# Performance work log

Hardware: AMD Instinct MI355X
Metric: run time of the kernel (lower is better)

Reference implementation:

```python
import jax, jax.numpy as jnp
import numpy as np

B, S, D, H = 2, 2048, 1024, 16
HD = D // H  # 64
LN_EPS = 1e-5


def setup_inputs() -> dict:
    key = jax.random.key(0)
    ks = jax.random.split(key, 5)
    hidden_states = jax.random.normal(ks[0], (B, S, D), dtype=jnp.float32)
    attention_mask = jnp.zeros((B, 1, 1, S), dtype=jnp.float32)  # additive mask
    # LayerNorm params
    ln_gamma = jnp.ones((D,), dtype=jnp.float32)
    ln_beta = jnp.zeros((D,), dtype=jnp.float32)
    # Q/K/V projections, no bias; stored as [in, out]
    sc = 1.0 / np.sqrt(D)
    Wq = jax.random.normal(ks[1], (D, D), dtype=jnp.float32) * sc
    Wk = jax.random.normal(ks[2], (D, D), dtype=jnp.float32) * sc
    Wv = jax.random.normal(ks[3], (D, D), dtype=jnp.float32) * sc
    return {"hidden_states": hidden_states, "attention_mask": attention_mask,
            "ln_gamma": ln_gamma, "ln_beta": ln_beta, "Wq": Wq, "Wk": Wk, "Wv": Wv}


def _layernorm(x, g, b):
    mu = jnp.mean(x, axis=-1, keepdims=True)
    var = jnp.mean(jnp.square(x - mu), axis=-1, keepdims=True)
    return (x - mu) * jax.lax.rsqrt(var + LN_EPS) * g + b


def reference(hidden_states, attention_mask, ln_gamma, ln_beta, Wq, Wk, Wv):
    h = _layernorm(hidden_states, ln_gamma, ln_beta)          # [B,S,D]
    # project and split heads: [B,S,D] -> [B,H,S,HD]
    def split_heads(x):
        return x.reshape(B, S, H, HD).transpose(0, 2, 1, 3)
    q = split_heads(h @ Wq)
    k = split_heads(h @ Wk)
    v = split_heads(h @ Wv)
    scores = jnp.einsum('bhqd,bhkd->bhqk', q, k) / jnp.sqrt(jnp.float32(HD))
    scores = scores + attention_mask                           # additive mask broadcast
    probs = jax.nn.softmax(scores, axis=-1)                    # dropout p=0 -> identity
    ctx = jnp.einsum('bhqk,bhkd->bhqd', probs, v)              # [B,H,S,HD]
    ctx = ctx.transpose(0, 2, 1, 3).reshape(B, S, H * HD)      # [B,S,D]
    return ctx
```

## Files before the change

kernel.cpp:

```cpp
#include <hip/hip_runtime.h>
#include <hip/hip_bf16.h>
#include <cstdint>

#define B_ 2
#define S_ 2048
#define D_ 1024
#define H_ 16
#define HD_ 64
#define M_ (B_*S_)

#define LOG2E 1.4426950408889634f
#define C1_ (0.125f * LOG2E)

typedef unsigned short u16;
typedef __bf16 bf16x8 __attribute__((ext_vector_type(8)));
typedef u16 u16x8 __attribute__((ext_vector_type(8)));
typedef float f32x4 __attribute__((ext_vector_type(4)));
typedef float f32x16 __attribute__((ext_vector_type(16)));
typedef int i32x4 __attribute__((ext_vector_type(4)));

static __device__ __forceinline__ u16 f2bu(float f) {
  __bf16 b = (__bf16)f;
  return __builtin_bit_cast(unsigned short, b);
}

static __device__ __forceinline__ int cvtpk(float a, float b) {
  int r;
  asm("v_cvt_pk_bf16_f32 %0, %1, %2" : "=v"(r) : "v"(a), "v"(b));
  return r;
}
static __device__ __forceinline__ void plswap(int &x, int &y) {
  asm("v_permlane32_swap_b32 %0, %1" : "+v"(x), "+v"(y));
}

#define GLOAD16(g, l) __builtin_amdgcn_global_load_lds( \
    (__attribute__((address_space(1))) void*)(g), \
    (__attribute__((address_space(3))) void*)(l), 16, 0, 0)

__global__ __launch_bounds__(256) void ln_kernel(const float* __restrict__ x,
    const float* __restrict__ g, const float* __restrict__ be, u16* __restrict__ h) {
  const int row = blockIdx.x;
  const int t = threadIdx.x;
  float4 v = reinterpret_cast<const float4*>(x + (size_t)row * D_)[t];
  float s = v.x + v.y + v.z + v.w;
  float sq = v.x*v.x + v.y*v.y + v.z*v.z + v.w*v.w;
  #pragma unroll
  for (int off = 32; off >= 1; off >>= 1) {
    s  += __shfl_down(s, off);
    sq += __shfl_down(sq, off);
  }
  __shared__ float red[8];
  const int wave = t >> 6, lane = t & 63;
  if (lane == 0) { red[wave] = s; red[4 + wave] = sq; }
  __syncthreads();
  if (t == 0) {
    float ts = red[0]+red[1]+red[2]+red[3];
    float tq = red[4]+red[5]+red[6]+red[7];
    float mu = ts * (1.0f / D_);
    red[0] = mu;
    red[1] = rsqrtf(tq * (1.0f / D_) - mu*mu + 1e-5f);
  }
  __syncthreads();
  const float mu = red[0], rs = red[1];
  float4 gg = reinterpret_cast<const float4*>(g)[t];
  float4 bb = reinterpret_cast<const float4*>(be)[t];
  ushort4 o;
  o.x = f2bu((v.x - mu) * rs * gg.x + bb.x);
  o.y = f2bu((v.y - mu) * rs * gg.y + bb.y);
  o.z = f2bu((v.z - mu) * rs * gg.z + bb.z);
  o.w = f2bu((v.w - mu) * rs * gg.w + bb.w);
  reinterpret_cast<ushort4*>(h + (size_t)row * D_)[t] = o;
}

__global__ __launch_bounds__(256) void wt_kernel(const float* __restrict__ W0,
    const float* __restrict__ W1, const float* __restrict__ W2, u16* __restrict__ wt) {
  const int z = blockIdx.z;
  const float* W = (z == 0) ? W0 : ((z == 1) ? W1 : W2);
  u16* out = wt + (size_t)z * D_ * D_;
  __shared__ float tile[32][33];
  const int n0 = blockIdx.x * 32, k0 = blockIdx.y * 32;
  const int tx = threadIdx.x, ty = threadIdx.y;
  #pragma unroll
  for (int j = 0; j < 4; ++j)
    tile[ty + 8*j][tx] = W[(size_t)(k0 + ty + 8*j) * D_ + n0 + tx];
  __syncthreads();
  #pragma unroll
  for (int j = 0; j < 4; ++j)
    out[(size_t)(n0 + ty + 8*j) * D_ + k0 + tx] = f2bu(tile[tx][ty + 8*j]);
}

__global__ __launch_bounds__(256) void qkv_gemm(const u16* __restrict__ hbuf,
    const u16* __restrict__ wt, u16* __restrict__ qkv) {
  const int z = blockIdx.z;
  const u16* Bt = wt + (size_t)z * D_ * D_;
  u16* outp = qkv + (size_t)z * (B_*H_*S_*HD_);
  __shared__ __align__(16) u16 As[128 * 32];
  __shared__ __align__(16) u16 Bs[128 * 32];
  const int t = threadIdx.x, lane = t & 63, wave = t >> 6;
  const int row0 = blockIdx.y * 128, col0 = blockIdx.x * 128;
  const int wm = wave >> 1, wn = wave & 1;
  f32x4 acc[4][4] = {};
  const int schunk = (t & 3) ^ ((t >> 3) & 3);
  const u16* ag = hbuf + (size_t)(row0 + (t >> 2)) * D_ + schunk * 8;
  const u16* bg = Bt   + (size_t)(col0 + (t >> 2)) * D_ + schunk * 8;
  u16* lA = &As[wave * 512];
  u16* lB = &Bs[wave * 512];
  const char* Ac = (const char*)As;
  const char* Bc = (const char*)Bs;
  const int cbase = (((lane >> 4) ^ ((lane >> 1) & 3)) << 4);

  for (int k0 = 0; k0 < D_; k0 += 32) {
    GLOAD16(ag + k0,           lA);
    GLOAD16(ag + k0 + 64 * D_, lA + 2048);
    GLOAD16(bg + k0,           lB);
    GLOAD16(bg + k0 + 64 * D_, lB + 2048);
    __syncthreads();
    bf16x8 af[4], bfr[4];
    #pragma unroll
    for (int m = 0; m < 4; ++m)
      af[m] = *reinterpret_cast<const bf16x8*>(Ac + (wm*64 + m*16 + (lane & 15)) * 64 + cbase);
    #pragma unroll
    for (int n = 0; n < 4; ++n)
      bfr[n] = *reinterpret_cast<const bf16x8*>(Bc + (wn*64 + n*16 + (lane & 15)) * 64 + cbase);
    #pragma unroll
    for (int m = 0; m < 4; ++m) {
      #pragma unroll
      for (int n = 0; n < 4; ++n)
        acc[m][n] = __builtin_amdgcn_mfma_f32_16x16x32_bf16(af[m], bfr[n], acc[m][n], 0, 0, 0);
    }
    __syncthreads();
  }
  #pragma unroll
  for (int m = 0; m < 4; ++m) {
    #pragma unroll
    for (int n = 0; n < 4; ++n) {
      const int gcol = col0 + wn*64 + n*16 + (lane & 15);
      const int hI = gcol >> 6, dI = gcol & 63;
      #pragma unroll
      for (int r = 0; r < 4; ++r) {
        const int grow = row0 + wm*64 + m*16 + (lane >> 4) * 4 + r;
        const int bI = grow >> 11, sI = grow & (S_ - 1);
        size_t idx;
        if (z == 2) idx = ((size_t)(bI * H_ + hI) * HD_ + dI) * S_ + sI;
        else        idx = ((size_t)(bI * H_ + hI) * S_ + sI) * HD_ + dI;
        outp[idx] = f2bu(acc[m][n][r]);
      }
    }
  }
}

static __device__ __forceinline__ void sm_pack(
    const f32x16& s, const float* __restrict__ mrow, int hf,
    float& dm, float& lsum, f32x16& o0, f32x16& o1,
    bf16x8& pfA, bf16x8& pfB) {
  float4 m0 = *reinterpret_cast<const float4*>(mrow + 4*hf);
  float4 m1 = *reinterpret_cast<const float4*>(mrow + 8 + 4*hf);
  float4 m2 = *reinterpret_cast<const float4*>(mrow + 16 + 4*hf);
  float4 m3 = *reinterpret_cast<const float4*>(mrow + 24 + 4*hf);
  float zb[16];
  #pragma unroll
  for (int r = 0; r < 4; ++r) {
    zb[r]      = s[r]      * C1_ + ((const float*)&m0)[r];
    zb[r + 4]  = s[r + 4]  * C1_ + ((const float*)&m1)[r];
    zb[r + 8]  = s[r + 8]  * C1_ + ((const float*)&m2)[r];
    zb[r + 12] = s[r + 12] * C1_ + ((const float*)&m3)[r];
  }
  float a0 = fmaxf(fmaxf(zb[0], zb[1]), zb[2]);
  float a1 = fmaxf(fmaxf(zb[3], zb[4]), zb[5]);
  float a2 = fmaxf(fmaxf(zb[6], zb[7]), zb[8]);
  float a3 = fmaxf(fmaxf(zb[9], zb[10]), zb[11]);
  float a4 = fmaxf(fmaxf(zb[12], zb[13]), zb[14]);
  float tm = fmaxf(fmaxf(fmaxf(a0, a1), fmaxf(a2, a3)), fmaxf(a4, zb[15]));
  tm = fmaxf(tm, __shfl_xor(tm, 32));
  if (__builtin_expect(__any(tm > dm + 8.0f), 0)) {
    float dnew = fmaxf(dm, tm - 8.0f);
    float sf = __builtin_amdgcn_exp2f(dm - dnew);
    lsum *= sf; o0 = o0 * sf; o1 = o1 * sf; dm = dnew;
  }
  float p[16];
  #pragma unroll
  for (int r = 0; r < 16; ++r) p[r] = __builtin_amdgcn_exp2f(zb[r] - dm);
  float s01 = (p[0] + p[1]) + (p[2] + p[3]);
  float s23 = (p[4] + p[5]) + (p[6] + p[7]);
  float s45 = (p[8] + p[9]) + (p[10] + p[11]);
  float s67 = (p[12] + p[13]) + (p[14] + p[15]);
  float rs = (s01 + s23) + (s45 + s67);
  rs += __shfl_xor(rs, 32);
  lsum += rs;
  int pk01 = cvtpk(p[0], p[1]),   pk23 = cvtpk(p[2], p[3]);
  int pk45 = cvtpk(p[4], p[5]),   pk67 = cvtpk(p[6], p[7]);
  int pk89 = cvtpk(p[8], p[9]),   pkAB = cvtpk(p[10], p[11]);
  int pkCD = cvtpk(p[12], p[13]), pkEF = cvtpk(p[14], p[15]);
  plswap(pk01, pk45); plswap(pk23, pk67);
  plswap(pk89, pkCD); plswap(pkAB, pkEF);
  i32x4 c0 = {pk01, pk23, pk45, pk67};
  i32x4 c1 = {pk89, pkAB, pkCD, pkEF};
  pfA = __builtin_bit_cast(bf16x8, c0);
  pfB = __builtin_bit_cast(bf16x8, c1);
}

__global__ __launch_bounds__(256, 2) void attn_kernel(const u16* __restrict__ qkv,
    const float* __restrict__ mask, float* __restrict__ out) {
  const int bid = blockIdx.x;
  const int x = bid & 7, rr = bid >> 3;
  const int j = rr & 15;
  const int pidx = x + ((rr >> 4) << 3);
  const int hI = pidx & 15, bI = pidx >> 4;
  const size_t plane = (size_t)pidx * (S_ * HD_);
  const u16* Qp  = qkv + plane;
  const u16* Kp  = qkv + (size_t)(B_*H_*S_*HD_) + plane;
  const u16* Vtp = qkv + 2*(size_t)(B_*H_*S_*HD_) + plane;

  const int t = threadIdx.x, lane = t & 63, wave = t >> 6;
  const int cl = lane & 31, hf = lane >> 5;
  const int swz = (cl & 7) << 4;

  __shared__ __align__(16) u16 KsBuf[2][64 * 64];
  __shared__ __align__(16) u16 VsBuf[2][64 * 64];
  __shared__ float maskLds[S_];

  #pragma unroll
  for (int i = 0; i < 2; ++i) {
    float4 mv = reinterpret_cast<const float4*>(mask + (size_t)bI * S_)[t + i*256];
    float4 sm = {mv.x * LOG2E - 8.0f, mv.y * LOG2E - 8.0f,
                 mv.z * LOG2E - 8.0f, mv.w * LOG2E - 8.0f};
    reinterpret_cast<float4*>(maskLds)[t + i*256] = sm;
  }

  const int q0 = j * 128 + wave * 32;
  bf16x8 qf[4];
  #pragma unroll
  for (int d = 0; d < 4; ++d)
    qf[d] = *reinterpret_cast<const bf16x8*>(
        Qp + (size_t)(q0 + cl) * HD_ + d * 16 + hf * 8);

  const int sr = t >> 3;
  const int scol = (((t & 7) * 16) ^ ((sr & 7) << 4)) >> 1;
  const u16* kSrc = Kp  + (size_t)sr * HD_ + scol;
  const u16* vSrc = Vtp + (size_t)sr * S_  + scol;
  const int L0 = wave * 512, L1 = 2048 + wave * 512;

  f32x16 oacc0 = {}, oacc1 = {};
  float dm = 0.f, lsum = 0.f;

  GLOAD16(kSrc,                  &KsBuf[0][L0]);
  GLOAD16(kSrc + 32 * HD_,       &KsBuf[0][L1]);
  GLOAD16(vSrc,                  &VsBuf[0][L0]);
  GLOAD16(vSrc + 32 * (size_t)S_, &VsBuf[0][L1]);
  int cur = 0;

  for (int kv0 = 0; kv0 < S_; kv0 += 64) {
    __syncthreads();
    if (kv0 + 64 < S_) {
      const u16* kn = kSrc + (size_t)(kv0 + 64) * HD_;
      const u16* vn = vSrc + (kv0 + 64);
      GLOAD16(kn,                   &KsBuf[cur ^ 1][L0]);
      GLOAD16(kn + 32 * HD_,        &KsBuf[cur ^ 1][L1]);
      GLOAD16(vn,                   &VsBuf[cur ^ 1][L0]);
      GLOAD16(vn + 32 * (size_t)S_, &VsBuf[cur ^ 1][L1]);
    }
    const char* Ks = (const char*)KsBuf[cur];
    const char* Vs = (const char*)VsBuf[cur];

    f32x16 s0 = {}, s1 = {};
    __builtin_amdgcn_s_setprio(1);
    #pragma unroll
    for (int d = 0; d < 4; ++d) {
      bf16x8 kf = *reinterpret_cast<const bf16x8*>(
          Ks + cl * 128 + ((d * 32 + hf * 16) ^ swz));
      s0 = __builtin_amdgcn_mfma_f32_32x32x16_bf16(kf, qf[d], s0, 0, 0, 0);
    }
    #pragma unroll
    for (int d = 0; d < 4; ++d) {
      bf16x8 kf = *reinterpret_cast<const bf16x8*>(
          Ks + (32 + cl) * 128 + ((d * 32 + hf * 16) ^ swz));
      s1 = __builtin_amdgcn_mfma_f32_32x32x16_bf16(kf, qf[d], s1, 0, 0, 0);
    }
    __builtin_amdgcn_s_setprio(0);

    bf16x8 pA, pB;
    sm_pack(s0, maskLds + kv0, hf, dm, lsum, oacc0, oacc1, pA, pB);
    __builtin_amdgcn_s_setprio(1);
    {
      bf16x8 vf;
      vf = *reinterpret_cast<const bf16x8*>(Vs + cl * 128 + ((hf * 16) ^ swz));
      oacc0 = __builtin_amdgcn_mfma_f32_32x32x16_bf16(vf, pA, oacc0, 0, 0, 0);
      vf = *reinterpret_cast<const bf16x8*>(Vs + (32 + cl) * 128 + ((hf * 16) ^ swz));
      oacc1 = __builtin_amdgcn_mfma_f32_32x32x16_bf16(vf, pA, oacc1, 0, 0, 0);
      vf = *reinterpret_cast<const bf16x8*>(Vs + cl * 128 + ((32 + hf * 16) ^ swz));
      oacc0 = __builtin_amdgcn_mfma_f32_32x32x16_bf16(vf, pB, oacc0, 0, 0, 0);
      vf = *reinterpret_cast<const bf16x8*>(Vs + (32 + cl) * 128 + ((32 + hf * 16) ^ swz));
      oacc1 = __builtin_amdgcn_mfma_f32_32x32x16_bf16(vf, pB, oacc1, 0, 0, 0);
    }
    __builtin_amdgcn_s_setprio(0);
    sm_pack(s1, maskLds + kv0 + 32, hf, dm, lsum, oacc0, oacc1, pA, pB);
    __builtin_amdgcn_s_setprio(1);
    {
      bf16x8 vf;
      vf = *reinterpret_cast<const bf16x8*>(Vs + cl * 128 + ((64 + hf * 16) ^ swz));
      oacc0 = __builtin_amdgcn_mfma_f32_32x32x16_bf16(vf, pA, oacc0, 0, 0, 0);
      vf = *reinterpret_cast<const bf16x8*>(Vs + (32 + cl) * 128 + ((64 + hf * 16) ^ swz));
      oacc1 = __builtin_amdgcn_mfma_f32_32x32x16_bf16(vf, pA, oacc1, 0, 0, 0);
      vf = *reinterpret_cast<const bf16x8*>(Vs + cl * 128 + ((96 + hf * 16) ^ swz));
      oacc0 = __builtin_amdgcn_mfma_f32_32x32x16_bf16(vf, pB, oacc0, 0, 0, 0);
      vf = *reinterpret_cast<const bf16x8*>(Vs + (32 + cl) * 128 + ((96 + hf * 16) ^ swz));
      oacc1 = __builtin_amdgcn_mfma_f32_32x32x16_bf16(vf, pB, oacc1, 0, 0, 0);
    }
    __builtin_amdgcn_s_setprio(0);
    cur ^= 1;
  }

  const float rinv = 1.0f / lsum;
  float* orow = out + ((size_t)bI * S_ + q0 + cl) * D_ + hI * HD_;
  #pragma unroll
  for (int jj = 0; jj < 4; ++jj) {
    float4 o0 = {oacc0[4*jj] * rinv, oacc0[4*jj+1] * rinv, oacc0[4*jj+2] * rinv, oacc0[4*jj+3] * rinv};
    float4 o1 = {oacc1[4*jj] * rinv, oacc1[4*jj+1] * rinv, oacc1[4*jj+2] * rinv, oacc1[4*jj+3] * rinv};
    *reinterpret_cast<float4*>(orow + 8*jj + 4*hf)      = o0;
    *reinterpret_cast<float4*>(orow + 32 + 8*jj + 4*hf) = o1;
  }
}

extern "C" void kernel_launch(void* const* d_in, const int* in_sizes, int n_in,
                              void* d_out, int out_size, void* d_ws, size_t ws_size,
                              hipStream_t stream) {
  const float* x     = (const float*)d_in[0];
  const float* mask  = (const float*)d_in[1];
  const float* gamma = (const float*)d_in[2];
  const float* beta  = (const float*)d_in[3];
  const float* Wq    = (const float*)d_in[4];
  const float* Wk    = (const float*)d_in[5];
  const float* Wv    = (const float*)d_in[6];
  float* out = (float*)d_out;

  char* ws = (char*)d_ws;
  u16* hbuf = (u16*)ws;
  u16* wt   = (u16*)(ws + (size_t)M_*D_*2);
  u16* qkv  = (u16*)(ws + (size_t)M_*D_*2 + 3ull*D_*D_*2);

  hipLaunchKernelGGL(ln_kernel, dim3(M_), dim3(256), 0, stream, x, gamma, beta, hbuf);
  hipLaunchKernelGGL(wt_kernel, dim3(32, 32, 3), dim3(32, 8), 0, stream, Wq, Wk, Wv, wt);
  hipLaunchKernelGGL(qkv_gemm, dim3(8, 32, 3), dim3(256), 0, stream, hbuf, wt, qkv);
  hipLaunchKernelGGL(attn_kernel, dim3(512), dim3(256), 0, stream, qkv, mask, out);
}
```

Measured before the change: 111.0 us.

## Load K/V fragments directly from global into registers, dropping LDS staging

The attention kernel no longer stages K and V tiles through double-buffered shared memory with per-iteration barriers. Each wave loads its own MFMA operand fragments straight from global memory, with K prefetched one tile ahead in registers. The softmax scale is folded into the Q projection epilogue, and the cross-half row-sum shuffle is deferred to the end, so it only runs when the rescale branch fires. This removes LDS traffic and barriers but raises register pressure and relies on cache hits for K/V reuse across the four waves.

```diff
diff --git a/kernel.cpp b/kernel.cpp
--- a/kernel.cpp
+++ b/kernel.cpp
@@ -130,6 +130,7 @@
     }
     __syncthreads();
   }
+  const float scl = (z == 0) ? C1_ : 1.0f;
   #pragma unroll
   for (int m = 0; m < 4; ++m) {
     #pragma unroll
@@ -143,27 +144,23 @@
         size_t idx;
         if (z == 2) idx = ((size_t)(bI * H_ + hI) * HD_ + dI) * S_ + sI;
         else        idx = ((size_t)(bI * H_ + hI) * S_ + sI) * HD_ + dI;
-        outp[idx] = f2bu(acc[m][n][r]);
+        outp[idx] = f2bu(acc[m][n][r] * scl);
       }
     }
   }
 }
 
 static __device__ __forceinline__ void sm_pack(
-    const f32x16& s, const float* __restrict__ mrow, int hf,
+    const f32x16& s, const float4* __restrict__ mk,
     float& dm, float& lsum, f32x16& o0, f32x16& o1,
     bf16x8& pfA, bf16x8& pfB) {
-  float4 m0 = *reinterpret_cast<const float4*>(mrow + 4*hf);
-  float4 m1 = *reinterpret_cast<const float4*>(mrow + 8 + 4*hf);
-  float4 m2 = *reinterpret_cast<const float4*>(mrow + 16 + 4*hf);
-  float4 m3 = *reinterpret_cast<const float4*>(mrow + 24 + 4*hf);
   float zb[16];
   #pragma unroll
   for (int r = 0; r < 4; ++r) {
-    zb[r]      = s[r]      * C1_ + ((const float*)&m0)[r];
-    zb[r + 4]  = s[r + 4]  * C1_ + ((const float*)&m1)[r];
-    zb[r + 8]  = s[r + 8]  * C1_ + ((const float*)&m2)[r];
-    zb[r + 12] = s[r + 12] * C1_ + ((const float*)&m3)[r];
+    zb[r]      = s[r]      + ((const float*)&mk[0])[r];
+    zb[r + 4]  = s[r + 4]  + ((const float*)&mk[1])[r];
+    zb[r + 8]  = s[r + 8]  + ((const float*)&mk[2])[r];
+    zb[r + 12] = s[r + 12] + ((const float*)&mk[3])[r];
   }
   float a0 = fmaxf(fmaxf(zb[0], zb[1]), zb[2]);
   float a1 = fmaxf(fmaxf(zb[3], zb[4]), zb[5]);
@@ -171,9 +168,9 @@
   float a3 = fmaxf(fmaxf(zb[9], zb[10]), zb[11]);
   float a4 = fmaxf(fmaxf(zb[12], zb[13]), zb[14]);
   float tm = fmaxf(fmaxf(fmaxf(a0, a1), fmaxf(a2, a3)), fmaxf(a4, zb[15]));
-  tm = fmaxf(tm, __shfl_xor(tm, 32));
   if (__builtin_expect(__any(tm > dm + 8.0f), 0)) {
-    float dnew = fmaxf(dm, tm - 8.0f);
+    float tp = fmaxf(tm, __shfl_xor(tm, 32));
+    float dnew = fmaxf(dm, tp - 8.0f);
     float sf = __builtin_amdgcn_exp2f(dm - dnew);
     lsum *= sf; o0 = o0 * sf; o1 = o1 * sf; dm = dnew;
   }
@@ -184,9 +181,7 @@
   float s23 = (p[4] + p[5]) + (p[6] + p[7]);
   float s45 = (p[8] + p[9]) + (p[10] + p[11]);
   float s67 = (p[12] + p[13]) + (p[14] + p[15]);
-  float rs = (s01 + s23) + (s45 + s67);
-  rs += __shfl_xor(rs, 32);
-  lsum += rs;
+  lsum += (s01 + s23) + (s45 + s67);
   int pk01 = cvtpk(p[0], p[1]),   pk23 = cvtpk(p[2], p[3]);
   int pk45 = cvtpk(p[4], p[5]),   pk67 = cvtpk(p[6], p[7]);
   int pk89 = cvtpk(p[8], p[9]),   pkAB = cvtpk(p[10], p[11]);
@@ -213,12 +208,8 @@
 
   const int t = threadIdx.x, lane = t & 63, wave = t >> 6;
   const int cl = lane & 31, hf = lane >> 5;
-  const int swz = (cl & 7) << 4;
-
-  __shared__ __align__(16) u16 KsBuf[2][64 * 64];
-  __shared__ __align__(16) u16 VsBuf[2][64 * 64];
+
   __shared__ float maskLds[S_];
-
   #pragma unroll
   for (int i = 0; i < 2; ++i) {
     float4 mv = reinterpret_cast<const float4*>(mask + (size_t)bI * S_)[t + i*256];
@@ -233,83 +224,77 @@
   for (int d = 0; d < 4; ++d)
     qf[d] = *reinterpret_cast<const bf16x8*>(
         Qp + (size_t)(q0 + cl) * HD_ + d * 16 + hf * 8);
-
-  const int sr = t >> 3;
-  const int scol = (((t & 7) * 16) ^ ((sr & 7) << 4)) >> 1;
-  const u16* kSrc = Kp  + (size_t)sr * HD_ + scol;
-  const u16* vSrc = Vtp + (size_t)sr * S_  + scol;
-  const int L0 = wave * 512, L1 = 2048 + wave * 512;
+  __syncthreads();
+
+  const u16* kbase = Kp  + (size_t)cl * HD_ + hf * 8;
+  const u16* vbase = Vtp + (size_t)cl * S_  + hf * 8;
 
   f32x16 oacc0 = {}, oacc1 = {};
   float dm = 0.f, lsum = 0.f;
 
-  GLOAD16(kSrc,                  &KsBuf[0][L0]);
-  GLOAD16(kSrc + 32 * HD_,       &KsBuf[0][L1]);
-  GLOAD16(vSrc,                  &VsBuf[0][L0]);
-  GLOAD16(vSrc + 32 * (size_t)S_, &VsBuf[0][L1]);
-  int cur = 0;
-
-  for (int kv0 = 0; kv0 < S_; kv0 += 64) {
-    __syncthreads();
-    if (kv0 + 64 < S_) {
-      const u16* kn = kSrc + (size_t)(kv0 + 64) * HD_;
-      const u16* vn = vSrc + (kv0 + 64);
-      GLOAD16(kn,                   &KsBuf[cur ^ 1][L0]);
-      GLOAD16(kn + 32 * HD_,        &KsBuf[cur ^ 1][L1]);
-      GLOAD16(vn,                   &VsBuf[cur ^ 1][L0]);
-      GLOAD16(vn + 32 * (size_t)S_, &VsBuf[cur ^ 1][L1]);
+  bf16x8 kf[2][8];
+  #pragma unroll
+  for (int s = 0; s < 2; ++s)
+    #pragma unroll
+    for (int d = 0; d < 4; ++d)
+      kf[0][s*4+d] = *reinterpret_cast<const bf16x8*>(kbase + (size_t)(s*32) * HD_ + d*16);
+
+  for (int it = 0; it < 16; ++it) {
+    #pragma unroll
+    for (int h = 0; h < 2; ++h) {
+      const int tt = 2*it + h;
+      const int kv0 = tt * 64;
+      float4 mk0[4], mk1[4];
+      #pragma unroll
+      for (int i = 0; i < 4; ++i) {
+        mk0[i] = *reinterpret_cast<const float4*>(&maskLds[kv0 + 8*i + 4*hf]);
+        mk1[i] = *reinterpret_cast<const float4*>(&maskLds[kv0 + 32 + 8*i + 4*hf]);
+      }
+      bf16x8 vf[8];
+      #pragma unroll
+      for (int s = 0; s < 2; ++s) {
+        vf[s*4+0] = *reinterpret_cast<const bf16x8*>(vbase + kv0 + s*32);
+        vf[s*4+1] = *reinterpret_cast<const bf16x8*>(vbase + 32*(size_t)S_ + kv0 + s*32);
+        vf[s*4+2] = *reinterpret_cast<const bf16x8*>(vbase + kv0 + s*32 + 16);
+        vf[s*4+3] = *reinterpret_cast<const bf16x8*>(vbase + 32*(size_t)S_ + kv0 + s*32 + 16);
+      }
+      f32x16 s0 = {}, s1 = {};
+      __builtin_amdgcn_s_setprio(1);
+      #pragma unroll
+      for (int d = 0; d < 4; ++d)
+        s0 = __builtin_amdgcn_mfma_f32_32x32x16_bf16(kf[h][d], qf[d], s0, 0, 0, 0);
+      #pragma unroll
+      for (int d = 0; d < 4; ++d)
+        s1 = __builtin_amdgcn_mfma_f32_32x32x16_bf16(kf[h][4+d], qf[d], s1, 0, 0, 0);
+      __builtin_amdgcn_s_setprio(0);
+      {
+        const int tn = (tt < 31) ? tt + 1 : 31;
+        const u16* kn = kbase + (size_t)(tn * 64) * HD_;
+        #pragma unroll
+        for (int s = 0; s < 2; ++s)
+          #pragma unroll
+          for (int d = 0; d < 4; ++d)
+            kf[h^1][s*4+d] = *reinterpret_cast<const bf16x8*>(kn + (size_t)(s*32) * HD_ + d*16);
+      }
+      bf16x8 pA, pB;
+      sm_pack(s0, mk0, dm, lsum, oacc0, oacc1, pA, pB);
+      __builtin_amdgcn_s_setprio(1);
+      oacc0 = __builtin_amdgcn_mfma_f32_32x32x16_bf16(vf[0], pA, oacc0, 0, 0, 0);
+      oacc1 = __builtin_amdgcn_mfma_f32_32x32x16_bf16(vf[1], pA, oacc1, 0, 0, 0);
+      oacc0 = __builtin_amdgcn_mfma_f32_32x32x16_bf16(vf[2], pB, oacc0, 0, 0, 0);
+      oacc1 = __builtin_amdgcn_mfma_f32_32x32x16_bf16(vf[3], pB, oacc1, 0, 0, 0);
+      __builtin_amdgcn_s_setprio(0);
+      sm_pack(s1, mk1, dm, lsum, oacc0, oacc1, pA, pB);
+      __builtin_amdgcn_s_setprio(1);
+      oacc0 = __builtin_amdgcn_mfma_f32_32x32x16_bf16(vf[4], pA, oacc0, 0, 0, 0);
+      oacc1 = __builtin_amdgcn_mfma_f32_32x32x16_bf16(vf[5], pA, oacc1, 0, 0, 0);
+      oacc0 = __builtin_amdgcn_mfma_f32_32x32x16_bf16(vf[6], pB, oacc0, 0, 0, 0);
+      oacc1 = __builtin_amdgcn_mfma_f32_32x32x16_bf16(vf[7], pB, oacc1, 0, 0, 0);
+      __builtin_amdgcn_s_setprio(0);
     }
-    const char* Ks = (const char*)KsBuf[cur];
-    const char* Vs = (const char*)VsBuf[cur];
-
-    f32x16 s0 = {}, s1 = {};
-    __builtin_amdgcn_s_setprio(1);
-    #pragma unroll
-    for (int d = 0; d < 4; ++d) {
-      bf16x8 kf = *reinterpret_cast<const bf16x8*>(
-          Ks + cl * 128 + ((d * 32 + hf * 16) ^ swz));
-      s0 = __builtin_amdgcn_mfma_f32_32x32x16_bf16(kf, qf[d], s0, 0, 0, 0);
-    }
-    #pragma unroll
-    for (int d = 0; d < 4; ++d) {
-      bf16x8 kf = *reinterpret_cast<const bf16x8*>(
-          Ks + (32 + cl) * 128 + ((d * 32 + hf * 16) ^ swz));
-      s1 = __builtin_amdgcn_mfma_f32_32x32x16_bf16(kf, qf[d], s1, 0, 0, 0);
-    }
-    __builtin_amdgcn_s_setprio(0);
-
-    bf16x8 pA, pB;
-    sm_pack(s0, maskLds + kv0, hf, dm, lsum, oacc0, oacc1, pA, pB);
-    __builtin_amdgcn_s_setprio(1);
-    {
-      bf16x8 vf;
-      vf = *reinterpret_cast<const bf16x8*>(Vs + cl * 128 + ((hf * 16) ^ swz));
-      oacc0 = __builtin_amdgcn_mfma_f32_32x32x16_bf16(vf, pA, oacc0, 0, 0, 0);
-      vf = *reinterpret_cast<const bf16x8*>(Vs + (32 + cl) * 128 + ((hf * 16) ^ swz));
-      oacc1 = __builtin_amdgcn_mfma_f32_32x32x16_bf16(vf, pA, oacc1, 0, 0, 0);
-      vf = *reinterpret_cast<const bf16x8*>(Vs + cl * 128 + ((32 + hf * 16) ^ swz));
-      oacc0 = __builtin_amdgcn_mfma_f32_32x32x16_bf16(vf, pB, oacc0, 0, 0, 0);
-      vf = *reinterpret_cast<const bf16x8*>(Vs + (32 + cl) * 128 + ((32 + hf * 16) ^ swz));
-      oacc1 = __builtin_amdgcn_mfma_f32_32x32x16_bf16(vf, pB, oacc1, 0, 0, 0);
-    }
-    __builtin_amdgcn_s_setprio(0);
-    sm_pack(s1, maskLds + kv0 + 32, hf, dm, lsum, oacc0, oacc1, pA, pB);
-    __builtin_amdgcn_s_setprio(1);
-    {
-      bf16x8 vf;
-      vf = *reinterpret_cast<const bf16x8*>(Vs + cl * 128 + ((64 + hf * 16) ^ swz));
-      oacc0 = __builtin_amdgcn_mfma_f32_32x32x16_bf16(vf, pA, oacc0, 0, 0, 0);
-      vf = *reinterpret_cast<const bf16x8*>(Vs + (32 + cl) * 128 + ((64 + hf * 16) ^ swz));
-      oacc1 = __builtin_amdgcn_mfma_f32_32x32x16_bf16(vf, pA, oacc1, 0, 0, 0);
-      vf = *reinterpret_cast<const bf16x8*>(Vs + cl * 128 + ((96 + hf * 16) ^ swz));
-      oacc0 = __builtin_amdgcn_mfma_f32_32x32x16_bf16(vf, pB, oacc0, 0, 0, 0);
-      vf = *reinterpret_cast<const bf16x8*>(Vs + (32 + cl) * 128 + ((96 + hf * 16) ^ swz));
-      oacc1 = __builtin_amdgcn_mfma_f32_32x32x16_bf16(vf, pB, oacc1, 0, 0, 0);
-    }
-    __builtin_amdgcn_s_setprio(0);
-    cur ^= 1;
-  }
-
+  }
+
+  lsum += __shfl_xor(lsum, 32);
   const float rinv = 1.0f / lsum;
   float* orow = out + ((size_t)bI * S_ + q0 + cl) * D_ + hI * HD_;
   #pragma unroll
```

New measurement: 169.9 us. 53.1% more time.
